# Kernel tuning notes

Hardware: AMD Instinct MI355X
Metric: run time of the kernel (lower is better)

Reference implementation:

```python
import jax, jax.numpy as jnp
import numpy as np

N_NODES = 50000
N_EDGES = 800000
INDIM = 128
HIDIM = 128
OUTDIM = 128


def setup_inputs() -> dict:
    key = jax.random.key(0)
    ks = jax.random.split(key, 12)
    x = jax.random.normal(ks[0], (N_NODES, INDIM), dtype=jnp.float32)
    edge_index = jax.random.randint(ks[1], (2, N_EDGES), 0, N_NODES, dtype=jnp.int64)
    edge_weights = jax.random.normal(ks[2], (N_EDGES, 1), dtype=jnp.float32)
    # GINEConv internal edge projection Linear(1 -> feat_dim) per layer
    We1 = jax.random.normal(ks[3], (1, INDIM), dtype=jnp.float32)
    be1 = jnp.zeros((INDIM,), dtype=jnp.float32)
    # layer MLPs (nn.Linear)
    W1 = jax.random.normal(ks[4], (INDIM, HIDIM), dtype=jnp.float32) / np.sqrt(INDIM)
    b1 = jnp.zeros((HIDIM,), dtype=jnp.float32)
    We2 = jax.random.normal(ks[5], (1, HIDIM), dtype=jnp.float32)
    be2 = jnp.zeros((HIDIM,), dtype=jnp.float32)
    W2 = jax.random.normal(ks[6], (HIDIM, OUTDIM), dtype=jnp.float32) / np.sqrt(HIDIM)
    b2 = jnp.zeros((OUTDIM,), dtype=jnp.float32)
    return {"x": x, "edge_index": edge_index, "edge_weights": edge_weights,
            "We1": We1, "be1": be1, "W1": W1, "b1": b1,
            "We2": We2, "be2": be2, "W2": W2, "b2": b2}


def _gine_conv(h, src, dst, edge_attr, We, be, W, b):
    # edge embedding: Linear(1 -> d)
    e = edge_attr @ We + be                     # [E, d]
    # message: relu(x_j + e_ij), gather from source nodes
    msg = jax.nn.relu(h[src] + e)               # [E, d]
    # scatter-sum aggregate at destination nodes
    agg = jax.ops.segment_sum(msg, dst, num_segments=N_NODES)  # [N, d]
    # (1 + eps) * x + aggr, eps = 0 (PyG default), then nn (Linear)
    return (h + agg) @ W + b


def reference(x, edge_index, edge_weights, We1, be1, W1, b1, We2, be2, W2, b2):
    src = edge_index[0]
    dst = edge_index[1]
    h = jax.nn.relu(_gine_conv(x, src, dst, edge_weights, We1, be1, W1, b1))
    out = _gine_conv(h, src, dst, edge_weights, We2, be2, W2, b2)
    return out
```

## Files before the change

### kernel.cpp

```cpp
#include <hip/hip_runtime.h>


typedef unsigned long long u64;
typedef unsigned int u32;
typedef unsigned short ushort;
typedef __attribute__((ext_vector_type(8))) short short8;
typedef __attribute__((ext_vector_type(4))) float f32x4;
typedef __attribute__((ext_vector_type(2))) float f32x2;
typedef __attribute__((ext_vector_type(4))) u32 u32x4;

constexpr int NN = 50000;
constexpr int NE = 800000;
constexpr int D  = 128;
constexpr int BSH = 6;
constexpr int NB  = (NN + 63) >> BSH;
constexpr int NC  = 128;
constexpr int CHUNK = NE / NC;
constexpr int BCAP = 4096;
constexpr int GR = 32;
constexpr int GG = (NN + GR - 1) / GR;
constexpr int NU4 = NN * D / 8;
constexpr int CPB = 1024;

__device__ __forceinline__ ushort f2bf(float f) {
    u32 u = __float_as_uint(f);
    return (ushort)((u + 0x7FFFu + ((u >> 16) & 1u)) >> 16);
}
__device__ __forceinline__ float bfl(u32 u) {
    return __uint_as_float(u << 16);
}
__device__ __forceinline__ float bfh(u32 u) {
    return __uint_as_float(u & 0xFFFF0000u);
}
__device__ __forceinline__ f32x2 unpk(u32 u) {
    f32x2 r; r.x = bfl(u); r.y = bfh(u); return r;
}
__device__ __forceinline__ u64 pack_edge(int src, int d6, float w) {
    return ((u64)__float_as_uint(w) << 32) | (u32)(src | (d6 << 17));
}


__global__ __launch_bounds__(256) void hist_w(
    const float* __restrict__ W1, const float* __restrict__ W2,
    ushort* __restrict__ Wt1, ushort* __restrict__ Wt2,
    const int* __restrict__ dst, int* __restrict__ G)
{
    int blk = blockIdx.x;
    if (blk < NC) {
        __shared__ int hh[NB];
        int t = threadIdx.x, c = blk;
        for (int i = t; i < NB; i += 256) hh[i] = 0;
        __syncthreads();
        int e0 = c * CHUNK;
        for (int i = t; i < CHUNK; i += 256)
            atomicAdd(&hh[dst[e0 + i] >> BSH], 1);
        __syncthreads();
        for (int i = t; i < NB; i += 256) G[c * NB + i] = hh[i];
    } else {
        int b = blk - NC;
        const float* W  = (b >= 4) ? W2 : W1;
        ushort*      Wt = (b >= 4) ? Wt2 : Wt1;
        int k0 = (b & 3) * 32;
        for (int i = threadIdx.x; i < 32 * D; i += 256) {
            int n = i >> 5, r = i & 31;
            Wt[n * D + k0 + r] = f2bf(W[(k0 + r) * D + n]);
        }
    }
}


__global__ __launch_bounds__(1024) void bucket_scatter(
    const int*   __restrict__ src,
    const int*   __restrict__ dst,
    const float* __restrict__ ew,
    const int*   __restrict__ G,
    int*         __restrict__ B,
    u64*         __restrict__ stage)
{
    __shared__ int base_s[NB];
    __shared__ int cnt_s[NB];
    __shared__ int pre_s[NB];
    __shared__ int tsum[1024];
    const int t = threadIdx.x, c = blockIdx.x;

    int S = 0, P = 0;
    if (t < NB) {
        #pragma unroll 8
        for (int cc = 0; cc < NC; ++cc) {
            int g = G[cc * NB + t];
            S += g;
            if (cc < c) P += g;
        }
        pre_s[t] = P;
    }
    tsum[t] = S;
    __syncthreads();

    for (int d = 1; d < 1024; d <<= 1) {
        int v = (t >= d) ? tsum[t - d] : 0;
        __syncthreads();
        tsum[t] += v;
        __syncthreads();
    }
    if (t < NB) base_s[t] = tsum[t] - S;
    __syncthreads();

    if (c == 0) {
        if (t < NB) B[t] = base_s[t];
        if (t == 0) B[NB] = NE;
    }
    if (t < NB) {
        base_s[t] += pre_s[t];
        cnt_s[t] = 0;
    }
    __syncthreads();

    int e0 = c * CHUNK;
    for (int i = t; i < CHUNK; i += 1024) {
        int e  = e0 + i;
        int d  = dst[e];
        int bk = d >> BSH;
        int r  = atomicAdd(&cnt_s[bk], 1);
        stage[base_s[bk] + r] = pack_edge(src[e], d & 63, ew[e]);
    }
}

__global__ __launch_bounds__(256) void bucket_csr_cast(
    const int* __restrict__ B, u64* __restrict__ stage, int* __restrict__ off,
    const float* __restrict__ x, ushort* __restrict__ xb)
{
    __shared__ u64 buf[BCAP];
    __shared__ int cnt[64];
    __shared__ int cur[64];
    __shared__ int noff[64];
    int t = threadIdx.x, b = blockIdx.x;

    #pragma unroll
    for (int j = 0; j < CPB / 256; ++j) {
        int i = b * CPB + j * 256 + t;
        if (i < NU4) {
            int base = i * 8;
            float4 a = *(const float4*)(x + base);
            float4 c = *(const float4*)(x + base + 4);
            uint4 o;
            o.x = (u32)f2bf(a.x) | ((u32)f2bf(a.y) << 16);
            o.y = (u32)f2bf(a.z) | ((u32)f2bf(a.w) << 16);
            o.z = (u32)f2bf(c.x) | ((u32)f2bf(c.y) << 16);
            o.w = (u32)f2bf(c.z) | ((u32)f2bf(c.w) << 16);
            *(uint4*)(xb + base) = o;
        }
    }

    int e0 = B[b], e1 = B[b + 1];
    int n = e1 - e0;
    if (n > BCAP) n = BCAP;
    if (t < 64) { cnt[t] = 0; cur[t] = 0; }
    __syncthreads();
    for (int i = t; i < n; i += 256)
        atomicAdd(&cnt[(int)((stage[e0 + i] >> 17) & 63)], 1);
    __syncthreads();
    if (t == 0) {
        int run = 0;
        for (int j = 0; j < 64; ++j) { noff[j] = run; run += cnt[j]; }
    }
    __syncthreads();
    int n0 = b << BSH;
    if (t < 64 && (n0 + t) < NN) off[n0 + t] = e0 + noff[t];
    if (b == NB - 1 && t == 0) off[NN] = NE;
    for (int i = t; i < n; i += 256) {
        u64 p = stage[e0 + i];
        int d6 = (int)((p >> 17) & 63);
        int r = atomicAdd(&cur[d6], 1);
        buf[noff[d6] + r] = p;
    }
    __syncthreads();
    for (int i = t; i < n; i += 256) stage[e0 + i] = buf[i];
}


__global__ __launch_bounds__(256, 4) void gine_layer(
    const ushort* __restrict__ hb,
    const int*    __restrict__ off,
    const u64*    __restrict__ epk,
    const float*  __restrict__ We,
    const float*  __restrict__ be,
    const ushort* __restrict__ Wtb,
    const float*  __restrict__ bias,
    float*        __restrict__ outf,
    ushort*       __restrict__ outb,
    int relu)
{
    __shared__ ushort As[GR * 140];

    const int t    = threadIdx.x;
    const int row0 = blockIdx.x * GR;

    const int g  = t >> 4;
    const int d8 = (t & 15) << 3;

    f32x2 wv[4], bv[4];
    #pragma unroll
    for (int j = 0; j < 4; ++j) {
        wv[j] = *(const f32x2*)(We + d8 + 2 * j);
        bv[j] = *(const f32x2*)(be + d8 + 2 * j);
    }
    const f32x2 zero2 = {0.f, 0.f};

    for (int nrep = 0; nrep < GR / 16; ++nrep) {
        int ln = nrep * 16 + g;
        int n  = row0 + ln;
        f32x2 a[4] = {zero2, zero2, zero2, zero2};
        if (n < NN) {
            u32x4 sv = *(const u32x4*)(hb + (size_t)n * D + d8);
            int e0 = off[n], e1 = off[n + 1];
            u64 p[8];
            int m0 = e1 - e0; if (m0 > 8) m0 = 8;
            #pragma unroll
            for (int k = 0; k < 8; ++k) p[k] = (k < m0) ? epk[e0 + k] : 0;
            for (int e = e0; e < e1; e += 8) {
                int m = e1 - e; if (m > 8) m = 8;
                u32x4 hv[8];
                #pragma unroll
                for (int k = 0; k < 8; ++k)
                    hv[k] = *(const u32x4*)(hb + (size_t)(p[k] & 0x1FFFF) * D + d8);
                u64 pn[8];
                int mn = e1 - (e + 8); if (mn > 8) mn = 8;
                #pragma unroll
                for (int k = 0; k < 8; ++k)
                    pn[k] = (k < mn) ? epk[e + 8 + k] : 0;
                #pragma unroll
                for (int k = 0; k < 8; ++k) {
                    if (k < m) {
                        float w = __uint_as_float((u32)(p[k] >> 32));
                        f32x2 w2 = {w, w};
                        a[0] += __builtin_elementwise_max(zero2,
                                  unpk(hv[k].x) + __builtin_elementwise_fma(w2, wv[0], bv[0]));
                        a[1] += __builtin_elementwise_max(zero2,
                                  unpk(hv[k].y) + __builtin_elementwise_fma(w2, wv[1], bv[1]));
                        a[2] += __builtin_elementwise_max(zero2,
                                  unpk(hv[k].z) + __builtin_elementwise_fma(w2, wv[2], bv[2]));
                        a[3] += __builtin_elementwise_max(zero2,
                                  unpk(hv[k].w) + __builtin_elementwise_fma(w2, wv[3], bv[3]));
                    }
                }
                #pragma unroll
                for (int k = 0; k < 8; ++k) p[k] = pn[k];
            }
            a[0] += unpk(sv.x);
            a[1] += unpk(sv.y);
            a[2] += unpk(sv.z);
            a[3] += unpk(sv.w);
        }
        uint2 lo, hi;
        lo.x = (u32)f2bf(a[0].x) | ((u32)f2bf(a[0].y) << 16);
        lo.y = (u32)f2bf(a[1].x) | ((u32)f2bf(a[1].y) << 16);
        hi.x = (u32)f2bf(a[2].x) | ((u32)f2bf(a[2].y) << 16);
        hi.y = (u32)f2bf(a[3].x) | ((u32)f2bf(a[3].y) << 16);
        *(uint2*)&As[ln * 140 + d8]     = lo;
        *(uint2*)&As[ln * 140 + d8 + 4] = hi;
    }
    __syncthreads();

    const int wave = t >> 6;
    const int lane = t & 63;
    const int q    = lane >> 4;
    const int m    = lane & 15;
    const int wc   = wave * 32;

    f32x4 acc[2][2] = {};
    #pragma unroll
    for (int kb = 0; kb < 4; ++kb) {
        int ak = kb * 32 + q * 8;
        short8 af[2];
        #pragma unroll
        for (int rg = 0; rg < 2; ++rg)
            af[rg] = *(const short8*)&As[(rg * 16 + m) * 140 + ak];
        #pragma unroll
        for (int ct = 0; ct < 2; ++ct) {
            short8 bf = *(const short8*)(Wtb + (wc + ct * 16 + m) * D + ak);
            #pragma unroll
            for (int rg = 0; rg < 2; ++rg)
                acc[rg][ct] = __builtin_amdgcn_mfma_f32_16x16x32_bf16(
                    af[rg], bf, acc[rg][ct], 0, 0, 0);
        }
    }

    #pragma unroll
    for (int ct = 0; ct < 2; ++ct) {
        int col = wc + ct * 16 + m;
        float bc = bias[col];
        #pragma unroll
        for (int rg = 0; rg < 2; ++rg) {
            #pragma unroll
            for (int r = 0; r < 4; ++r) {
                int grow = row0 + rg * 16 + q * 4 + r;
                if (grow < NN) {
                    float v = acc[rg][ct][r] + bc;
                    if (relu) v = fmaxf(0.f, v);
                    if (outb) outb[(size_t)grow * D + col] = f2bf(v);
                    else __builtin_nontemporal_store(v, outf + (size_t)grow * D + col);
                }
            }
        }
    }
}

extern "C" void kernel_launch(void* const* d_in, const int* in_sizes, int n_in,
                              void* d_out, int out_size, void* d_ws, size_t ws_size,
                              hipStream_t stream)
{
    const float* x   = (const float*)d_in[0];
    const int*   ei  = (const int*)  d_in[1];
    const float* ew  = (const float*)d_in[2];
    const float* We1 = (const float*)d_in[3];
    const float* be1 = (const float*)d_in[4];
    const float* W1  = (const float*)d_in[5];
    const float* b1  = (const float*)d_in[6];
    const float* We2 = (const float*)d_in[7];
    const float* be2 = (const float*)d_in[8];
    const float* W2  = (const float*)d_in[9];
    const float* b2  = (const float*)d_in[10];

    float* out = (float*)d_out;

    ushort* xb   = (ushort*)d_ws;
    ushort* hb   = xb + (size_t)NN * D;
    ushort* Wt1  = hb + (size_t)NN * D;
    ushort* Wt2  = Wt1 + D * D;
    u64*   stage = (u64*)(Wt2 + D * D);
    int*   G     = (int*)(stage + NE);
    int*   B     = G + NC * NB;
    int*   off   = B + NB + 2;

    const int* src = ei;
    const int* dst = ei + NE;

    hist_w<<<NC + 8, 256, 0, stream>>>(W1, W2, Wt1, Wt2, dst, G);

    bucket_scatter<<<NC, 1024, 0, stream>>>(src, dst, ew, G, B, stage);
    bucket_csr_cast<<<NB, 256, 0, stream>>>(B, stage, off, x, xb);

    gine_layer<<<GG, 256, 0, stream>>>(xb, off, stage, We1, be1, Wt1, b1,
                                       nullptr, hb, 1);

    gine_layer<<<GG, 256, 0, stream>>>(hb, off, stage, We2, be2, Wt2, b2,
                                       out, nullptr, 0);
}
```

Baseline: 209.4 us.

## Fold per-node CSR sort into layer kernels and fuse the x cast into scatter

Drops the separate bucket_csr_cast kernel. Buckets shrink to 32 destination nodes so each gine_layer block owns exactly one bucket. That block loads its bucket's packed edges, counting-sorts them by local destination in shared memory, and reads neighbour lists from LDS instead of a global CSR offset array. The x-to-bf16 cast moves into the scatter kernel, whose prefix sum now covers two buckets per thread because there are more buckets. This removes a kernel launch and a global read-write pass over the edge array, at the cost of redoing the local sort in both layers and losing the register prefetch of the next edge batch.

```diff
diff --git a/kernel.cpp b/kernel.cpp
--- a/kernel.cpp
+++ b/kernel.cpp
@@ -12,15 +12,13 @@
 constexpr int NN = 50000;
 constexpr int NE = 800000;
 constexpr int D  = 128;
-constexpr int BSH = 6;
-constexpr int NB  = (NN + 63) >> BSH;
+constexpr int BSH = 5;
+constexpr int NB  = (NN + 31) >> BSH;
 constexpr int NC  = 128;
 constexpr int CHUNK = NE / NC;
-constexpr int BCAP = 4096;
+constexpr int BCAP = 1024;
 constexpr int GR = 32;
-constexpr int GG = (NN + GR - 1) / GR;
 constexpr int NU4 = NN * D / 8;
-constexpr int CPB = 1024;
 
 __device__ __forceinline__ ushort f2bf(float f) {
     u32 u = __float_as_uint(f);
@@ -35,8 +33,8 @@
 __device__ __forceinline__ f32x2 unpk(u32 u) {
     f32x2 r; r.x = bfl(u); r.y = bfh(u); return r;
 }
-__device__ __forceinline__ u64 pack_edge(int src, int d6, float w) {
-    return ((u64)__float_as_uint(w) << 32) | (u32)(src | (d6 << 17));
+__device__ __forceinline__ u64 pack_edge(int src, int d5, float w) {
+    return ((u64)__float_as_uint(w) << 32) | (u32)(src | (d5 << 17));
 }
 
 
@@ -69,31 +67,56 @@
 }
 
 
-__global__ __launch_bounds__(1024) void bucket_scatter(
+__global__ __launch_bounds__(1024) void scatter_cast(
     const int*   __restrict__ src,
     const int*   __restrict__ dst,
     const float* __restrict__ ew,
     const int*   __restrict__ G,
     int*         __restrict__ B,
-    u64*         __restrict__ stage)
+    u64*         __restrict__ stage,
+    const float* __restrict__ x,
+    ushort*      __restrict__ xb)
 {
     __shared__ int base_s[NB];
     __shared__ int cnt_s[NB];
-    __shared__ int pre_s[NB];
     __shared__ int tsum[1024];
     const int t = threadIdx.x, c = blockIdx.x;
-
-    int S = 0, P = 0;
-    if (t < NB) {
+    const int b0 = 2 * t, b1 = 2 * t + 1;
+
+    int S0 = 0, P0 = 0, S1 = 0, P1 = 0;
+    if (b0 < NB) {
         #pragma unroll 8
         for (int cc = 0; cc < NC; ++cc) {
-            int g = G[cc * NB + t];
-            S += g;
-            if (cc < c) P += g;
-        }
-        pre_s[t] = P;
-    }
-    tsum[t] = S;
+            int g = G[cc * NB + b0];
+            S0 += g;
+            if (cc < c) P0 += g;
+        }
+    }
+    if (b1 < NB) {
+        #pragma unroll 8
+        for (int cc = 0; cc < NC; ++cc) {
+            int g = G[cc * NB + b1];
+            S1 += g;
+            if (cc < c) P1 += g;
+        }
+    }
+    tsum[t] = S0 + S1;
+
+    #pragma unroll
+    for (int j = 0; j < 7; ++j) {
+        int i = (c + j * NC) * 1024 + t;
+        if (i < NU4) {
+            int base = i * 8;
+            float4 a = *(const float4*)(x + base);
+            float4 d = *(const float4*)(x + base + 4);
+            uint4 o;
+            o.x = (u32)f2bf(a.x) | ((u32)f2bf(a.y) << 16);
+            o.y = (u32)f2bf(a.z) | ((u32)f2bf(a.w) << 16);
+            o.z = (u32)f2bf(d.x) | ((u32)f2bf(d.y) << 16);
+            o.w = (u32)f2bf(d.z) | ((u32)f2bf(d.w) << 16);
+            *(uint4*)(xb + base) = o;
+        }
+    }
     __syncthreads();
 
     for (int d = 1; d < 1024; d <<= 1) {
@@ -102,16 +125,20 @@
         tsum[t] += v;
         __syncthreads();
     }
-    if (t < NB) base_s[t] = tsum[t] - S;
-    __syncthreads();
-
+    int pairbase = tsum[t] - (S0 + S1);
+
+    if (b0 < NB) {
+        base_s[b0] = pairbase + P0;
+        cnt_s[b0] = 0;
+    }
+    if (b1 < NB) {
+        base_s[b1] = pairbase + S0 + P1;
+        cnt_s[b1] = 0;
+    }
     if (c == 0) {
-        if (t < NB) B[t] = base_s[t];
-        if (t == 0) B[NB] = NE;
-    }
-    if (t < NB) {
-        base_s[t] += pre_s[t];
-        cnt_s[t] = 0;
+        if (b0 < NB) B[b0] = pairbase;
+        if (b1 < NB) B[b1] = pairbase + S0;
+        if (t == 0)  B[NB] = NE;
     }
     __syncthreads();
 
@@ -121,66 +148,14 @@
         int d  = dst[e];
         int bk = d >> BSH;
         int r  = atomicAdd(&cnt_s[bk], 1);
-        stage[base_s[bk] + r] = pack_edge(src[e], d & 63, ew[e]);
-    }
-}
-
-__global__ __launch_bounds__(256) void bucket_csr_cast(
-    const int* __restrict__ B, u64* __restrict__ stage, int* __restrict__ off,
-    const float* __restrict__ x, ushort* __restrict__ xb)
-{
-    __shared__ u64 buf[BCAP];
-    __shared__ int cnt[64];
-    __shared__ int cur[64];
-    __shared__ int noff[64];
-    int t = threadIdx.x, b = blockIdx.x;
-
-    #pragma unroll
-    for (int j = 0; j < CPB / 256; ++j) {
-        int i = b * CPB + j * 256 + t;
-        if (i < NU4) {
-            int base = i * 8;
-            float4 a = *(const float4*)(x + base);
-            float4 c = *(const float4*)(x + base + 4);
-            uint4 o;
-            o.x = (u32)f2bf(a.x) | ((u32)f2bf(a.y) << 16);
-            o.y = (u32)f2bf(a.z) | ((u32)f2bf(a.w) << 16);
-            o.z = (u32)f2bf(c.x) | ((u32)f2bf(c.y) << 16);
-            o.w = (u32)f2bf(c.z) | ((u32)f2bf(c.w) << 16);
-            *(uint4*)(xb + base) = o;
-        }
-    }
-
-    int e0 = B[b], e1 = B[b + 1];
-    int n = e1 - e0;
-    if (n > BCAP) n = BCAP;
-    if (t < 64) { cnt[t] = 0; cur[t] = 0; }
-    __syncthreads();
-    for (int i = t; i < n; i += 256)
-        atomicAdd(&cnt[(int)((stage[e0 + i] >> 17) & 63)], 1);
-    __syncthreads();
-    if (t == 0) {
-        int run = 0;
-        for (int j = 0; j < 64; ++j) { noff[j] = run; run += cnt[j]; }
-    }
-    __syncthreads();
-    int n0 = b << BSH;
-    if (t < 64 && (n0 + t) < NN) off[n0 + t] = e0 + noff[t];
-    if (b == NB - 1 && t == 0) off[NN] = NE;
-    for (int i = t; i < n; i += 256) {
-        u64 p = stage[e0 + i];
-        int d6 = (int)((p >> 17) & 63);
-        int r = atomicAdd(&cur[d6], 1);
-        buf[noff[d6] + r] = p;
-    }
-    __syncthreads();
-    for (int i = t; i < n; i += 256) stage[e0 + i] = buf[i];
+        stage[base_s[bk] + r] = pack_edge(src[e], d & 31, ew[e]);
+    }
 }
 
 
 __global__ __launch_bounds__(256, 4) void gine_layer(
     const ushort* __restrict__ hb,
-    const int*    __restrict__ off,
+    const int*    __restrict__ B,
     const u64*    __restrict__ epk,
     const float*  __restrict__ We,
     const float*  __restrict__ be,
@@ -190,10 +165,41 @@
     ushort*       __restrict__ outb,
     int relu)
 {
-    __shared__ ushort As[GR * 140];
+    __shared__ u64 As64[GR * 140 / 4];
+    __shared__ u64 buf[BCAP];
+    __shared__ int cnt[32];
+    __shared__ int noff[32];
+    __shared__ int cur[32];
+    ushort* As = (ushort*)As64;
 
     const int t    = threadIdx.x;
-    const int row0 = blockIdx.x * GR;
+    const int b    = blockIdx.x;
+    const int row0 = b << BSH;
+
+    int e0 = B[b];
+    int n  = B[b + 1] - e0;
+    if (n > BCAP) n = BCAP;
+    if (t < 32) { cnt[t] = 0; cur[t] = 0; }
+    __syncthreads();
+    for (int i = t; i < n; i += 256) {
+        u64 p = epk[e0 + i];
+        As64[i] = p;
+        atomicAdd(&cnt[(int)((p >> 17) & 31)], 1);
+    }
+    __syncthreads();
+    if (t == 0) {
+        int run = 0;
+        #pragma unroll
+        for (int j = 0; j < 32; ++j) { noff[j] = run; run += cnt[j]; }
+    }
+    __syncthreads();
+    for (int i = t; i < n; i += 256) {
+        u64 p = As64[i];
+        int d5 = (int)((p >> 17) & 31);
+        int r = atomicAdd(&cur[d5], 1);
+        buf[noff[d5] + r] = p;
+    }
+    __syncthreads();
 
     const int g  = t >> 4;
     const int d8 = (t & 15) << 3;
@@ -208,26 +214,20 @@
 
     for (int nrep = 0; nrep < GR / 16; ++nrep) {
         int ln = nrep * 16 + g;
-        int n  = row0 + ln;
+        int nd = row0 + ln;
         f32x2 a[4] = {zero2, zero2, zero2, zero2};
-        if (n < NN) {
-            u32x4 sv = *(const u32x4*)(hb + (size_t)n * D + d8);
-            int e0 = off[n], e1 = off[n + 1];
-            u64 p[8];
-            int m0 = e1 - e0; if (m0 > 8) m0 = 8;
-            #pragma unroll
-            for (int k = 0; k < 8; ++k) p[k] = (k < m0) ? epk[e0 + k] : 0;
-            for (int e = e0; e < e1; e += 8) {
-                int m = e1 - e; if (m > 8) m = 8;
+        if (nd < NN) {
+            u32x4 sv = *(const u32x4*)(hb + (size_t)nd * D + d8);
+            int s = noff[ln], deg = cnt[ln];
+            for (int e = 0; e < deg; e += 8) {
+                int m = deg - e; if (m > 8) m = 8;
+                u64 p[8];
+                #pragma unroll
+                for (int k = 0; k < 8; ++k) p[k] = (k < m) ? buf[s + e + k] : 0;
                 u32x4 hv[8];
                 #pragma unroll
                 for (int k = 0; k < 8; ++k)
                     hv[k] = *(const u32x4*)(hb + (size_t)(p[k] & 0x1FFFF) * D + d8);
-                u64 pn[8];
-                int mn = e1 - (e + 8); if (mn > 8) mn = 8;
-                #pragma unroll
-                for (int k = 0; k < 8; ++k)
-                    pn[k] = (k < mn) ? epk[e + 8 + k] : 0;
                 #pragma unroll
                 for (int k = 0; k < 8; ++k) {
                     if (k < m) {
@@ -243,8 +243,6 @@
                                   unpk(hv[k].w) + __builtin_elementwise_fma(w2, wv[3], bv[3]));
                     }
                 }
-                #pragma unroll
-                for (int k = 0; k < 8; ++k) p[k] = pn[k];
             }
             a[0] += unpk(sv.x);
             a[1] += unpk(sv.y);
@@ -330,19 +328,17 @@
     u64*   stage = (u64*)(Wt2 + D * D);
     int*   G     = (int*)(stage + NE);
     int*   B     = G + NC * NB;
-    int*   off   = B + NB + 2;
 
     const int* src = ei;
     const int* dst = ei + NE;
 
     hist_w<<<NC + 8, 256, 0, stream>>>(W1, W2, Wt1, Wt2, dst, G);
 
-    bucket_scatter<<<NC, 1024, 0, stream>>>(src, dst, ew, G, B, stage);
-    bucket_csr_cast<<<NB, 256, 0, stream>>>(B, stage, off, x, xb);
-
-    gine_layer<<<GG, 256, 0, stream>>>(xb, off, stage, We1, be1, Wt1, b1,
+    scatter_cast<<<NC, 1024, 0, stream>>>(src, dst, ew, G, B, stage, x, xb);
+
+    gine_layer<<<NB, 256, 0, stream>>>(xb, B, stage, We1, be1, Wt1, b1,
                                        nullptr, hb, 1);
 
-    gine_layer<<<GG, 256, 0, stream>>>(hb, off, stage, We2, be2, Wt2, b2,
+    gine_layer<<<NB, 256, 0, stream>>>(hb, B, stage, We2, be2, Wt2, b2,
                                        out, nullptr, 0);
 }
```

Measured after the change: 223.9 us. +6.9%, slower.

## Split bucket prefix scan into dedicated kernels and widen scatter to more chunks

Applied to the files above, without the earlier changes.

Raises the number of edge chunks from 128 to 512 so that the histogram and scatter kernels fill more compute units. Each scatter block used to recompute column sums over all chunk histograms and run its own block-wide scan. That redundant prefix work now happens once, in a new wave-parallel column scan kernel plus a single-block scan over bucket totals. The fp32-to-bf16 cast of x moves from the CSR kernel into the scatter kernel. The cost is two extra kernel launches and a larger per-chunk prefix table, and the CSR kernel loses its cast work.

```diff
diff --git a/kernel.cpp b/kernel.cpp
--- a/kernel.cpp
+++ b/kernel.cpp
@@ -14,13 +14,12 @@
 constexpr int D  = 128;
 constexpr int BSH = 6;
 constexpr int NB  = (NN + 63) >> BSH;
-constexpr int NC  = 128;
-constexpr int CHUNK = NE / NC;
+constexpr int NC  = 512;
+constexpr int CHUNK = (NE + NC - 1) / NC;
 constexpr int BCAP = 4096;
 constexpr int GR = 32;
 constexpr int GG = (NN + GR - 1) / GR;
 constexpr int NU4 = NN * D / 8;
-constexpr int CPB = 1024;
 
 __device__ __forceinline__ ushort f2bf(float f) {
     u32 u = __float_as_uint(f);
@@ -52,8 +51,10 @@
         for (int i = t; i < NB; i += 256) hh[i] = 0;
         __syncthreads();
         int e0 = c * CHUNK;
-        for (int i = t; i < CHUNK; i += 256)
-            atomicAdd(&hh[dst[e0 + i] >> BSH], 1);
+        for (int i = t; i < CHUNK; i += 256) {
+            int e = e0 + i;
+            if (e < NE) atomicAdd(&hh[dst[e] >> BSH], 1);
+        }
         __syncthreads();
         for (int i = t; i < NB; i += 256) G[c * NB + i] = hh[i];
     } else {
@@ -69,88 +70,109 @@
 }
 
 
+__global__ __launch_bounds__(256) void colscan(
+    const int* __restrict__ G, int* __restrict__ P, int* __restrict__ S)
+{
+    int wv = (blockIdx.x * 256 + threadIdx.x) >> 6;
+    int l  = threadIdx.x & 63;
+    if (wv >= NB) return;
+    int g[8];
+    int s = 0;
+    #pragma unroll
+    for (int j = 0; j < 8; ++j) {
+        g[j] = G[(l * 8 + j) * NB + wv];
+        s += g[j];
+    }
+    int incl = s;
+    #pragma unroll
+    for (int d = 1; d < 64; d <<= 1) {
+        int v = __shfl_up(incl, d, 64);
+        if (l >= d) incl += v;
+    }
+    int pre = incl - s;
+    #pragma unroll
+    for (int j = 0; j < 8; ++j) {
+        P[(size_t)wv * NC + l * 8 + j] = pre;
+        pre += g[j];
+    }
+    if (l == 63) S[wv] = incl;
+}
+
+
+__global__ __launch_bounds__(1024) void basescan(
+    const int* __restrict__ S, int* __restrict__ B)
+{
+    __shared__ int ts[1024];
+    int t = threadIdx.x;
+    int v = (t < NB) ? S[t] : 0;
+    ts[t] = v;
+    __syncthreads();
+    for (int d = 1; d < 1024; d <<= 1) {
+        int u = (t >= d) ? ts[t - d] : 0;
+        __syncthreads();
+        ts[t] += u;
+        __syncthreads();
+    }
+    if (t < NB) B[t] = ts[t] - v;
+    if (t == 0) B[NB] = NE;
+}
+
+
 __global__ __launch_bounds__(1024) void bucket_scatter(
     const int*   __restrict__ src,
     const int*   __restrict__ dst,
     const float* __restrict__ ew,
-    const int*   __restrict__ G,
-    int*         __restrict__ B,
-    u64*         __restrict__ stage)
+    const int*   __restrict__ P,
+    const int*   __restrict__ B,
+    u64*         __restrict__ stage,
+    const float* __restrict__ x,
+    ushort*      __restrict__ xb)
 {
     __shared__ int base_s[NB];
     __shared__ int cnt_s[NB];
-    __shared__ int pre_s[NB];
-    __shared__ int tsum[1024];
     const int t = threadIdx.x, c = blockIdx.x;
 
-    int S = 0, P = 0;
-    if (t < NB) {
-        #pragma unroll 8
-        for (int cc = 0; cc < NC; ++cc) {
-            int g = G[cc * NB + t];
-            S += g;
-            if (cc < c) P += g;
-        }
-        pre_s[t] = P;
-    }
-    tsum[t] = S;
-    __syncthreads();
-
-    for (int d = 1; d < 1024; d <<= 1) {
-        int v = (t >= d) ? tsum[t - d] : 0;
-        __syncthreads();
-        tsum[t] += v;
-        __syncthreads();
-    }
-    if (t < NB) base_s[t] = tsum[t] - S;
-    __syncthreads();
-
-    if (c == 0) {
-        if (t < NB) B[t] = base_s[t];
-        if (t == 0) B[NB] = NE;
-    }
-    if (t < NB) {
-        base_s[t] += pre_s[t];
-        cnt_s[t] = 0;
+    for (int b = t; b < NB; b += 1024) {
+        base_s[b] = B[b] + P[(size_t)b * NC + c];
+        cnt_s[b] = 0;
+    }
+
+    for (int i = t; i < CHUNK; i += 1024) {
+        int u = c * CHUNK + i;
+        if (u < NU4) {
+            int base = u * 8;
+            float4 a = *(const float4*)(x + base);
+            float4 d = *(const float4*)(x + base + 4);
+            uint4 o;
+            o.x = (u32)f2bf(a.x) | ((u32)f2bf(a.y) << 16);
+            o.y = (u32)f2bf(a.z) | ((u32)f2bf(a.w) << 16);
+            o.z = (u32)f2bf(d.x) | ((u32)f2bf(d.y) << 16);
+            o.w = (u32)f2bf(d.z) | ((u32)f2bf(d.w) << 16);
+            *(uint4*)(xb + base) = o;
+        }
     }
     __syncthreads();
 
     int e0 = c * CHUNK;
     for (int i = t; i < CHUNK; i += 1024) {
-        int e  = e0 + i;
-        int d  = dst[e];
-        int bk = d >> BSH;
-        int r  = atomicAdd(&cnt_s[bk], 1);
-        stage[base_s[bk] + r] = pack_edge(src[e], d & 63, ew[e]);
-    }
-}
-
-__global__ __launch_bounds__(256) void bucket_csr_cast(
-    const int* __restrict__ B, u64* __restrict__ stage, int* __restrict__ off,
-    const float* __restrict__ x, ushort* __restrict__ xb)
+        int e = e0 + i;
+        if (e < NE) {
+            int d  = dst[e];
+            int bk = d >> BSH;
+            int r  = atomicAdd(&cnt_s[bk], 1);
+            stage[base_s[bk] + r] = pack_edge(src[e], d & 63, ew[e]);
+        }
+    }
+}
+
+__global__ __launch_bounds__(256) void bucket_csr(
+    const int* __restrict__ B, u64* __restrict__ stage, int* __restrict__ off)
 {
     __shared__ u64 buf[BCAP];
     __shared__ int cnt[64];
     __shared__ int cur[64];
     __shared__ int noff[64];
     int t = threadIdx.x, b = blockIdx.x;
-
-    #pragma unroll
-    for (int j = 0; j < CPB / 256; ++j) {
-        int i = b * CPB + j * 256 + t;
-        if (i < NU4) {
-            int base = i * 8;
-            float4 a = *(const float4*)(x + base);
-            float4 c = *(const float4*)(x + base + 4);
-            uint4 o;
-            o.x = (u32)f2bf(a.x) | ((u32)f2bf(a.y) << 16);
-            o.y = (u32)f2bf(a.z) | ((u32)f2bf(a.w) << 16);
-            o.z = (u32)f2bf(c.x) | ((u32)f2bf(c.y) << 16);
-            o.w = (u32)f2bf(c.z) | ((u32)f2bf(c.w) << 16);
-            *(uint4*)(xb + base) = o;
-        }
-    }
-
     int e0 = B[b], e1 = B[b + 1];
     int n = e1 - e0;
     if (n > BCAP) n = BCAP;
@@ -329,16 +351,19 @@
     ushort* Wt2  = Wt1 + D * D;
     u64*   stage = (u64*)(Wt2 + D * D);
     int*   G     = (int*)(stage + NE);
-    int*   B     = G + NC * NB;
+    int*   P     = G + (size_t)NC * NB;
+    int*   S     = P + (size_t)NB * NC;
+    int*   B     = S + NB;
     int*   off   = B + NB + 2;
 
     const int* src = ei;
     const int* dst = ei + NE;
 
     hist_w<<<NC + 8, 256, 0, stream>>>(W1, W2, Wt1, Wt2, dst, G);
-
-    bucket_scatter<<<NC, 1024, 0, stream>>>(src, dst, ew, G, B, stage);
-    bucket_csr_cast<<<NB, 256, 0, stream>>>(B, stage, off, x, xb);
+    colscan<<<(NB * 64 + 255) / 256, 256, 0, stream>>>(G, P, S);
+    basescan<<<1, 1024, 0, stream>>>(S, B);
+    bucket_scatter<<<NC, 1024, 0, stream>>>(src, dst, ew, P, B, stage, x, xb);
+    bucket_csr<<<NB, 256, 0, stream>>>(B, stage, off);
 
     gine_layer<<<GG, 256, 0, stream>>>(xb, off, stage, We1, be1, Wt1, b1,
                                        nullptr, hb, 1);
```

New measurement: 211.5 us. Within noise of the previous version (+1.0%).
